# Kernel tuning notes

Measured on AMD Instinct MI355X. Metric: run time of the kernel, lower is better.

The kernel has to match this reference:

```python
import jax, jax.numpy as jnp
import numpy as np

TEMPERATURE = 0.1
EPS = 1e-8  # torch F.cosine_similarity norm clamp


def setup_inputs() -> dict:
    key = jax.random.key(0)
    k1, k2 = jax.random.split(key)
    N, D, N_CLASSES = 4096, 512, 16
    features = jax.random.normal(k1, (N, D), dtype=jnp.float32)
    labels = jax.random.randint(k2, (N,), 0, N_CLASSES, dtype=jnp.int64)
    return {"features": features, "labels": labels}


def reference(features, labels):
    N = features.shape[0]
    # cosine similarity via normalize + matmul (same math as the broadcasted
    # F.cosine_similarity, expressed as a BLAS path)
    norms = jnp.clip(jnp.linalg.norm(features, axis=1, keepdims=True), EPS)
    f = features / norms
    sim = f @ f.T  # (N, N)

    # drop the diagonal: row i keeps columns j != i, giving (N, N-1)
    j = jnp.arange(N - 1)
    cols = j[None, :] + (j[None, :] >= jnp.arange(N)[:, None])  # (N, N-1)
    sim_nd = jnp.take_along_axis(sim, cols, axis=1)

    # positive mask: same label, diagonal excluded, same column layout
    eq = labels[:, None] == labels[None, :]
    pos_nd = jnp.take_along_axis(eq, cols, axis=1)  # (N, N-1) bool

    logits = sim_nd / TEMPERATURE
    # torch.max(mask.float(), dim=1) -> first positive index per row
    targets = jnp.argmax(pos_nd.astype(jnp.float32), axis=1)  # (N,)

    logp = jax.nn.log_softmax(logits, axis=1)
    loss = -jnp.mean(jnp.take_along_axis(logp, targets[:, None], axis=1))
    return loss
```

## Files before the change

### kernel.cpp

```cpp
#include <hip/hip_runtime.h>
#include <hip/hip_bf16.h>
#include <math.h>

#define NROW 4096
#define DIM  512
#define TINV8 0.0390625f
#define EPSN 1e-8f
#define BT 64
#define NB (NROW / BT)
#define NBLK (NB * (NB + 1) / 2)
#define SLOTS (2 * NB)

typedef float f32x4 __attribute__((ext_vector_type(4)));

__device__ __forceinline__ void gload_lds16(const void* g, void* l) {
    __builtin_amdgcn_global_load_lds(
        (const __attribute__((address_space(1))) unsigned int*)g,
        (__attribute__((address_space(3))) unsigned int*)l,
        16, 0, 0);
}

__global__ __launch_bounds__(256) void kprep(const float* __restrict__ feat,
                                             const int* __restrict__ labels,
                                             unsigned char* __restrict__ fb8,
                                             int* __restrict__ target,
                                             int* __restrict__ donecnt) {
    if (blockIdx.x < NROW / 4) {
        const int row  = blockIdx.x * 4 + (threadIdx.x >> 6);
        const int lane = threadIdx.x & 63;
        const float* rp = feat + (size_t)row * DIM + lane * 8;
        float4 v0 = *(const float4*)rp;
        float4 v1 = *(const float4*)(rp + 4);
        float ss = v0.x*v0.x + v0.y*v0.y + v0.z*v0.z + v0.w*v0.w
                 + v1.x*v1.x + v1.y*v1.y + v1.z*v1.z + v1.w*v1.w;
        #pragma unroll
        for (int m = 1; m < 64; m <<= 1) ss += __shfl_xor(ss, m);
        const float inv = 16.0f / fmaxf(sqrtf(ss), EPSN);
        int w0 = __builtin_amdgcn_cvt_pk_fp8_f32(v0.x * inv, v0.y * inv, 0, false);
        w0     = __builtin_amdgcn_cvt_pk_fp8_f32(v0.z * inv, v0.w * inv, w0, true);
        int w1 = __builtin_amdgcn_cvt_pk_fp8_f32(v1.x * inv, v1.y * inv, 0, false);
        w1     = __builtin_amdgcn_cvt_pk_fp8_f32(v1.z * inv, v1.w * inv, w1, true);
        *(int2*)(fb8 + (size_t)row * DIM + lane * 8) = make_int2(w0, w1);
    } else {
        __shared__ int firstS[16], secondS[16];
        const int t = threadIdx.x;
        if (t < 16) { firstS[t] = NROW; secondS[t] = NROW; }
        if (t == 0)
            __hip_atomic_store(donecnt, 0, __ATOMIC_RELAXED, __HIP_MEMORY_SCOPE_AGENT);
        __syncthreads();
        for (int i = t; i < NROW; i += 256) atomicMin(&firstS[labels[i]], i);
        __syncthreads();
        for (int i = t; i < NROW; i += 256) {
            const int c = labels[i];
            if (i != firstS[c]) atomicMin(&secondS[c], i);
        }
        __syncthreads();
        for (int i = t; i < NROW; i += 256) {
            const int c = labels[i];
            int tg = (firstS[c] == i) ? secondS[c] : firstS[c];
            if (tg >= NROW) tg = (i == 0) ? 1 : 0;
            target[i] = tg;
        }
    }
}

__global__ __launch_bounds__(256, 8) void ksim(const unsigned char* __restrict__ fb8,
                                               const int* __restrict__ target,
                                               float* __restrict__ tlog,
                                               float* __restrict__ psums) {
    __shared__ __align__(16) unsigned char As[2][BT * 64];
    __shared__ __align__(16) unsigned char Bs[2][BT * 64];

    const int idx = blockIdx.x;
    int bi = (int)((129.0f - sqrtf(16641.0f - 8.0f * (float)idx)) * 0.5f);
    #define TRIOFF(b) ((b) * (129 - (b)) / 2)
    while (TRIOFF(bi + 1) <= idx) ++bi;
    while (TRIOFF(bi) > idx) --bi;
    const int bj = bi + (idx - TRIOFF(bi));
    const bool offdiag = (bi != bj);

    const int brow = bi * BT;
    const int bcol = bj * BT;
    const int tid  = threadIdx.x;
    const int wid  = tid >> 6;
    const int lane = tid & 63;
    const int wm = wid >> 1, wn = wid & 1;

    f32x4 acc[2][2];
    #pragma unroll
    for (int m = 0; m < 2; m++)
        #pragma unroll
        for (int n = 0; n < 2; n++)
            #pragma unroll
            for (int q = 0; q < 4; q++) acc[m][n][q] = 0.0f;

    const int skey = ((lane >> 2) & 3) ^ ((lane >> 4) & 3);
    const int sc   = (lane & 3) ^ skey;
    const int srow = wid * 16 + (lane >> 2);

    auto STAGE = [&](int buf, int kb) {
        const unsigned char* gA = fb8 + (size_t)(brow + srow) * DIM + kb + sc * 16;
        gload_lds16(gA, &As[buf][(wid * 16) * 64]);
        if (offdiag) {
            const unsigned char* gB = fb8 + (size_t)(bcol + srow) * DIM + kb + sc * 16;
            gload_lds16(gB, &Bs[buf][(wid * 16) * 64]);
        }
    };

    const int ro   = lane & 15;
    const int rkey = (ro & 3) ^ ((ro >> 2) & 3);
    const int hp   = (lane >> 4) & 1;
    const int g2   = lane >> 5;

    int cur = 0;
    STAGE(cur, 0);
    __syncthreads();

    for (int t = 0; t < DIM / 64; ++t) {
        if (t + 1 < DIM / 64) STAGE(cur ^ 1, (t + 1) * 64);
        const unsigned char* Ab = As[cur];
        const unsigned char* Bb = offdiag ? Bs[cur] : As[cur];
        #pragma unroll
        for (int kk = 0; kk < 2; kk++) {
            const int p   = (kk * 2 + g2) ^ rkey;
            const int cof = (p * 2 + hp) * 8;
            long a[2], b[2];
            #pragma unroll
            for (int m = 0; m < 2; m++)
                a[m] = *(const long*)(Ab + (wm * 32 + m * 16 + ro) * 64 + cof);
            #pragma unroll
            for (int n = 0; n < 2; n++)
                b[n] = *(const long*)(Bb + (wn * 32 + n * 16 + ro) * 64 + cof);
            #pragma unroll
            for (int m = 0; m < 2; m++)
                #pragma unroll
                for (int n = 0; n < 2; n++)
                    acc[m][n] = __builtin_amdgcn_mfma_f32_16x16x32_fp8_fp8(a[m], b[n], acc[m][n], 0, 0, 0);
        }
        __syncthreads();
        cur ^= 1;
    }

    const int lhi = lane >> 4, llo = lane & 15;
    float colacc[2] = {0.f, 0.f};
    int tgj[2] = {-1, -1};
    if (offdiag) {
        #pragma unroll
        for (int n = 0; n < 2; n++) tgj[n] = target[bcol + wn * 32 + n * 16 + llo];
    }

    #pragma unroll
    for (int m = 0; m < 2; m++) {
        #pragma unroll
        for (int q = 0; q < 4; q++) {
            const int i  = brow + wm * 32 + m * 16 + lhi * 4 + q;
            const int tgi = target[i];
            float psum = 0.0f;
            #pragma unroll
            for (int n = 0; n < 2; n++) {
                const int j = bcol + wn * 32 + n * 16 + llo;
                const float logit = acc[m][n][q] * TINV8;
                const float expv  = __expf(logit);
                if (j != i) psum += expv;
                if (j == tgi) tlog[i] = logit;
                if (offdiag) {
                    colacc[n] += expv;
                    if (i == tgj[n]) tlog[j] = logit;
                }
            }
            psum += __shfl_xor(psum, 1);
            psum += __shfl_xor(psum, 2);
            psum += __shfl_xor(psum, 4);
            psum += __shfl_xor(psum, 8);
            if (llo == 0) psums[(size_t)(2 * bj + wn) * NROW + i] = psum;
        }
    }
    if (offdiag) {
        #pragma unroll
        for (int n = 0; n < 2; n++) {
            colacc[n] += __shfl_xor(colacc[n], 16);
            colacc[n] += __shfl_xor(colacc[n], 32);
            if (lhi == 0)
                psums[(size_t)(2 * bi + wm) * NROW + bcol + wn * 32 + n * 16 + llo] = colacc[n];
        }
    }
}

__global__ __launch_bounds__(256) void kloss(const float* __restrict__ psums,
                                             const float* __restrict__ tlog,
                                             float* __restrict__ ploss,
                                             int* __restrict__ donecnt,
                                             float* __restrict__ out) {
    const int tid = threadIdx.x;
    const int r   = tid & 63;
    const int w   = tid >> 6;
    const int brow = blockIdx.x * BT;

    float a = 0.0f;
    for (int s = w; s < SLOTS; s += 4)
        a += psums[(size_t)s * NROW + brow + r];
    __shared__ float red[256];
    red[tid] = a;
    __syncthreads();

    if (tid < 64) {
        const float tot = red[tid] + red[tid + 64] + red[tid + 128] + red[tid + 192];
        float partial = __logf(tot) - tlog[brow + tid];
        #pragma unroll
        for (int m = 1; m < 64; m <<= 1) partial += __shfl_xor(partial, m);
        if (tid == 0)
            __hip_atomic_store(&ploss[blockIdx.x], partial, __ATOMIC_RELAXED, __HIP_MEMORY_SCOPE_AGENT);
    }

    asm volatile("s_waitcnt vmcnt(0)" ::: "memory");
    __shared__ int lastS;
    if (tid == 0)
        lastS = (__hip_atomic_fetch_add(donecnt, 1, __ATOMIC_RELAXED, __HIP_MEMORY_SCOPE_AGENT) == NB - 1);
    __syncthreads();
    if (!lastS) return;

    if (tid < 64) {
        float v = __hip_atomic_load(&ploss[tid], __ATOMIC_RELAXED, __HIP_MEMORY_SCOPE_AGENT);
        #pragma unroll
        for (int m = 1; m < 64; m <<= 1) v += __shfl_xor(v, m);
        if (tid == 0) out[0] = v / (float)NROW;
    }
}

extern "C" void kernel_launch(void* const* d_in, const int* in_sizes, int n_in,
                              void* d_out, int out_size, void* d_ws, size_t ws_size,
                              hipStream_t stream) {
    const float* feat  = (const float*)d_in[0];
    const int* labels  = (const int*)d_in[1];
    float* out = (float*)d_out;

    char* ws = (char*)d_ws;
    unsigned char* fb8 = (unsigned char*)ws;
    float* psums  = (float*)(ws + (size_t)NROW * DIM);
    float* tlog   = (float*)(ws + 2 * (size_t)NROW * DIM);
    int*   target = (int*)(tlog + NROW);
    float* ploss  = (float*)(target + NROW);
    int*   donecnt = (int*)(ploss + NB);

    kprep<<<NROW / 4 + 1, 256, 0, stream>>>(feat, labels, fb8, target, donecnt);
    ksim <<<NBLK, 256, 0, stream>>>(fb8, target, tlog, psums);
    kloss<<<NB, 256, 0, stream>>>(psums, tlog, ploss, donecnt, out);
}
```

Measured before the change: 44.63 us.

## Load MFMA fragments directly from global memory instead of staging through LDS

Removes the double-buffered LDS staging (global_load_lds plus swizzled reads and per-step barriers) and has each wave load its 8-byte fp8 fragments straight from global memory, with a one-step register prefetch. This drops the block-wide synchronisation and LDS traffic. In exchange, operands shared by multiple waves are now read redundantly from global/L2, and the loads are narrow 8-byte accesses with row strides.

```diff
diff --git a/kernel.cpp b/kernel.cpp
--- a/kernel.cpp
+++ b/kernel.cpp
@@ -12,13 +12,6 @@
 #define SLOTS (2 * NB)
 
 typedef float f32x4 __attribute__((ext_vector_type(4)));
-
-__device__ __forceinline__ void gload_lds16(const void* g, void* l) {
-    __builtin_amdgcn_global_load_lds(
-        (const __attribute__((address_space(1))) unsigned int*)g,
-        (__attribute__((address_space(3))) unsigned int*)l,
-        16, 0, 0);
-}
 
 __global__ __launch_bounds__(256) void kprep(const float* __restrict__ feat,
                                              const int* __restrict__ labels,
@@ -68,9 +61,6 @@
                                                const int* __restrict__ target,
                                                float* __restrict__ tlog,
                                                float* __restrict__ psums) {
-    __shared__ __align__(16) unsigned char As[2][BT * 64];
-    __shared__ __align__(16) unsigned char Bs[2][BT * 64];
-
     const int idx = blockIdx.x;
     int bi = (int)((129.0f - sqrtf(16641.0f - 8.0f * (float)idx)) * 0.5f);
     #define TRIOFF(b) ((b) * (129 - (b)) / 2)
@@ -86,6 +76,12 @@
     const int lane = tid & 63;
     const int wm = wid >> 1, wn = wid & 1;
 
+    const int fr = lane & 15;
+    const int k8 = (lane >> 4) * 8;
+
+    const unsigned char* Abase = fb8 + (size_t)(brow + wm * 32 + fr) * DIM + k8;
+    const unsigned char* Bbase = fb8 + (size_t)(bcol + wn * 32 + fr) * DIM + k8;
+
     f32x4 acc[2][2];
     #pragma unroll
     for (int m = 0; m < 2; m++)
@@ -94,51 +90,30 @@
             #pragma unroll
             for (int q = 0; q < 4; q++) acc[m][n][q] = 0.0f;
 
-    const int skey = ((lane >> 2) & 3) ^ ((lane >> 4) & 3);
-    const int sc   = (lane & 3) ^ skey;
-    const int srow = wid * 16 + (lane >> 2);
-
-    auto STAGE = [&](int buf, int kb) {
-        const unsigned char* gA = fb8 + (size_t)(brow + srow) * DIM + kb + sc * 16;
-        gload_lds16(gA, &As[buf][(wid * 16) * 64]);
-        if (offdiag) {
-            const unsigned char* gB = fb8 + (size_t)(bcol + srow) * DIM + kb + sc * 16;
-            gload_lds16(gB, &Bs[buf][(wid * 16) * 64]);
-        }
-    };
-
-    const int ro   = lane & 15;
-    const int rkey = (ro & 3) ^ ((ro >> 2) & 3);
-    const int hp   = (lane >> 4) & 1;
-    const int g2   = lane >> 5;
-
-    int cur = 0;
-    STAGE(cur, 0);
-    __syncthreads();
-
-    for (int t = 0; t < DIM / 64; ++t) {
-        if (t + 1 < DIM / 64) STAGE(cur ^ 1, (t + 1) * 64);
-        const unsigned char* Ab = As[cur];
-        const unsigned char* Bb = offdiag ? Bs[cur] : As[cur];
-        #pragma unroll
-        for (int kk = 0; kk < 2; kk++) {
-            const int p   = (kk * 2 + g2) ^ rkey;
-            const int cof = (p * 2 + hp) * 8;
-            long a[2], b[2];
-            #pragma unroll
-            for (int m = 0; m < 2; m++)
-                a[m] = *(const long*)(Ab + (wm * 32 + m * 16 + ro) * 64 + cof);
+    long a0[2], b0[2], a1[2], b1[2];
+    #pragma unroll
+    for (int m = 0; m < 2; m++) {
+        a0[m] = *(const long*)(Abase + m * 16 * DIM);
+        b0[m] = *(const long*)(Bbase + m * 16 * DIM);
+    }
+
+    #pragma unroll
+    for (int t = 0; t < 16; ++t) {
+        if (t < 15) {
+            const int kn = (t + 1) * 32;
+            #pragma unroll
+            for (int m = 0; m < 2; m++) {
+                a1[m] = *(const long*)(Abase + kn + m * 16 * DIM);
+                b1[m] = *(const long*)(Bbase + kn + m * 16 * DIM);
+            }
+        }
+        #pragma unroll
+        for (int m = 0; m < 2; m++)
             #pragma unroll
             for (int n = 0; n < 2; n++)
-                b[n] = *(const long*)(Bb + (wn * 32 + n * 16 + ro) * 64 + cof);
-            #pragma unroll
-            for (int m = 0; m < 2; m++)
-                #pragma unroll
-                for (int n = 0; n < 2; n++)
-                    acc[m][n] = __builtin_amdgcn_mfma_f32_16x16x32_fp8_fp8(a[m], b[n], acc[m][n], 0, 0, 0);
-        }
-        __syncthreads();
-        cur ^= 1;
+                acc[m][n] = __builtin_amdgcn_mfma_f32_16x16x32_fp8_fp8(a0[m], b0[n], acc[m][n], 0, 0, 0);
+        #pragma unroll
+        for (int m = 0; m < 2; m++) { a0[m] = a1[m]; b0[m] = b1[m]; }
     }
 
     const int lhi = lane >> 4, llo = lane & 15;
```

Measured after the change: 94.08 us. 111% more time.
